# Performance work log

Measured on AMD Instinct MI355X. Metric: run time of the kernel, lower is better.

## Reference

```python
import jax, jax.numpy as jnp
import numpy as np

K = 16  # number of neighbors (init kwarg k)
N_POINTS = 8_000_000
D_FEAT = 6


def setup_inputs() -> dict:
    key = jax.random.key(0)
    k1, k2, k3 = jax.random.split(key, 3)
    P = jax.random.normal(k1, (N_POINTS, D_FEAT), dtype=jnp.float32)
    W = jax.random.normal(k2, (3, 10), dtype=jnp.float32) * 0.1  # nn.Linear(10, 3) weight
    b = jax.random.normal(k3, (3,), dtype=jnp.float32) * 0.1     # nn.Linear(10, 3) bias
    i = 12345
    return {"P": P, "W": W, "b": b, "i": i}


def reference(P, W, b, i):
    # --- knn(i): note torch .topk defaults to largest=True, so this faithfully
    # selects the K points with the LARGEST distance to point i.
    pi = P[i, :3]                                   # [3]
    d = jnp.linalg.norm(P[:, :3] - pi, axis=1)      # [N] streaming distance pass
    _, idx = jax.lax.top_k(d, K)                    # [K]
    near = P[idx]                                   # [K, D]
    nloc = near[:, :3]                              # [K, 3]

    # --- rel_pos_enc, vectorized over all K neighbors (one tiny GEMM)
    diff = pi[None, :] - nloc                       # [K, 3]
    dist = jnp.linalg.norm(diff, axis=1, keepdims=True)  # [K, 1]
    feat = jnp.concatenate(
        [jnp.broadcast_to(pi, (K, 3)), nloc, diff, dist], axis=1
    )                                               # [K, 10]
    R = feat @ W.T + b                              # [K, 3]

    # --- forward: concat neighbor coords with encoding
    return jnp.concatenate([nloc, R], axis=1)       # [K, 6]
```

## Files before the change

kernel.cpp:

```cpp
#include <hip/hip_runtime.h>
#include <math.h>

#define KTOP 16
#define T1   256
#define B1   2048
#define PTS_PER_TILE 512
#define F4_PER_TILE  768
#define T2   1024
#define NC2  (B1 * KTOP)

typedef unsigned long long ull;

__device__ __forceinline__ ull pack_key(float d, unsigned idx) {
    return ((ull)__float_as_uint(d) << 32) | (ull)(0xFFFFFFFFu - idx);
}

__device__ __forceinline__ void insert_key(ull (&k)[KTOP], ull key) {
    ull t = key;
#pragma unroll
    for (int j = 0; j < KTOP; ++j) {
        const ull a = k[j];
        const bool c = (t > a);
        k[j] = c ? t : a;
        t    = c ? a : t;
    }
}

__device__ __forceinline__ float dist3(float x, float y, float z,
                                       float px, float py, float pz) {
#pragma clang fp contract(off)
    const float dx = x - px;
    const float dy = y - py;
    const float dz = z - pz;
    const float s  = (dx * dx + dy * dy) + dz * dz;
    return sqrtf(s);
}

__global__ __launch_bounds__(T1, 4) void pass1_topk(const float* __restrict__ P,
                                                    const int*   __restrict__ ipq,
                                                    int n,
                                                    ull* __restrict__ cand) {
    __shared__ float4 tile_f4[F4_PER_TILE];

    const int tid = threadIdx.x;

    const int i0 = ipq[0];
    const float pix = P[6 * i0 + 0];
    const float piy = P[6 * i0 + 1];
    const float piz = P[6 * i0 + 2];

    ull k[KTOP];
#pragma unroll
    for (int j = 0; j < KTOP; ++j) k[j] = 0ull;

    const float4* __restrict__ P4 = (const float4*)P;
    const int nTiles = n / PTS_PER_TILE;

    int tile = blockIdx.x;
    float4 r0, r1, r2;
    if (tile < nTiles) {
        const int b = tile * F4_PER_TILE + tid;
        r0 = P4[b];
        r1 = P4[b + T1];
        r2 = P4[b + 2 * T1];
    }

    for (; tile < nTiles; tile += B1) {
        __syncthreads();
        tile_f4[tid]          = r0;
        tile_f4[tid + T1]     = r1;
        tile_f4[tid + 2 * T1] = r2;
        const int next = tile + B1;
        if (next < nTiles) {
            const int b = next * F4_PER_TILE + tid;
            r0 = P4[b];
            r1 = P4[b + T1];
            r2 = P4[b + 2 * T1];
        }
        __syncthreads();

        const float* lp = (const float*)tile_f4 + 12 * tid;
        const float x0 = lp[0], y0 = lp[1],  z0 = lp[2];
        const float x1 = lp[6], y1 = lp[7],  z1 = lp[8];
        const unsigned id0 = (unsigned)(tile * PTS_PER_TILE + 2 * tid);
        const float d0 = dist3(x0, y0, z0, pix, piy, piz);
        const float d1 = dist3(x1, y1, z1, pix, piy, piz);
        const ull k0 = pack_key(d0, id0);
        const ull k1 = pack_key(d1, id0 + 1);
        if (k0 > k[KTOP - 1]) insert_key(k, k0);
        if (k1 > k[KTOP - 1]) insert_key(k, k1);
    }

    for (int p = nTiles * PTS_PER_TILE + blockIdx.x * T1 + tid; p < n; p += B1 * T1) {
        const float d = dist3(P[6 * p], P[6 * p + 1], P[6 * p + 2], pix, piy, piz);
        const ull key = pack_key(d, (unsigned)p);
        if (key > k[KTOP - 1]) insert_key(k, key);
    }

    __shared__ ull s_w[T1 / 64];
    __shared__ ull s_best;
    const int lane = tid & 63;
    const int wid  = tid >> 6;

    for (int r = 0; r < KTOP; ++r) {
        const ull mk = k[0];
        ull rv = mk;
#pragma unroll
        for (int m = 32; m >= 1; m >>= 1) {
            const ull ov = __shfl_xor(rv, m);
            if (ov > rv) rv = ov;
        }
        if (lane == 0) s_w[wid] = rv;
        __syncthreads();
        if (tid == 0) {
            ull b = s_w[0];
            for (int w = 1; w < T1 / 64; ++w) if (s_w[w] > b) b = s_w[w];
            s_best = b;
            cand[blockIdx.x * KTOP + r] = b;
        }
        __syncthreads();
        if (mk == s_best) {
#pragma unroll
            for (int j = 0; j < KTOP - 1; ++j) k[j] = k[j + 1];
            k[KTOP - 1] = 0ull;
        }
    }
}

__global__ __launch_bounds__(T2, 1) void pass2_final(const float* __restrict__ P,
                                                     const int*   __restrict__ ipq,
                                                     const float* __restrict__ W,
                                                     const float* __restrict__ bvec,
                                                     const ull*   __restrict__ cand,
                                                     float* __restrict__ out) {
    __shared__ ull s_w[T2 / 64];
    __shared__ ull s_best;
    __shared__ ull s_final[KTOP];

    const int tid  = threadIdx.x;
    const int lane = tid & 63;
    const int wid  = tid >> 6;

    ull k[KTOP];
#pragma unroll
    for (int j = 0; j < KTOP; ++j) k[j] = 0ull;

    for (int c = tid; c < NC2; c += T2) {
        const ull key = cand[c];
        if (key > k[KTOP - 1]) insert_key(k, key);
    }

    for (int r = 0; r < KTOP; ++r) {
        const ull mk = k[0];
        ull rv = mk;
#pragma unroll
        for (int m = 32; m >= 1; m >>= 1) {
            const ull ov = __shfl_xor(rv, m);
            if (ov > rv) rv = ov;
        }
        if (lane == 0) s_w[wid] = rv;
        __syncthreads();
        if (tid == 0) {
            ull b = s_w[0];
            for (int w = 1; w < T2 / 64; ++w) if (s_w[w] > b) b = s_w[w];
            s_best = b;
            s_final[r] = b;
        }
        __syncthreads();
        if (mk == s_best) {
#pragma unroll
            for (int j = 0; j < KTOP - 1; ++j) k[j] = k[j + 1];
            k[KTOP - 1] = 0ull;
        }
    }
    __syncthreads();

    if (tid < KTOP) {
        const ull kk = s_final[tid];
        const float d = __uint_as_float((unsigned)(kk >> 32));
        const unsigned idx = 0xFFFFFFFFu - (unsigned)(kk & 0xFFFFFFFFull);
        const int   i0  = ipq[0];
        const float pix = P[6 * i0 + 0], piy = P[6 * i0 + 1], piz = P[6 * i0 + 2];
        const float nx  = P[6 * (size_t)idx + 0];
        const float ny  = P[6 * (size_t)idx + 1];
        const float nz  = P[6 * (size_t)idx + 2];
        float dx, dy, dz;
        {
#pragma clang fp contract(off)
            dx = pix - nx; dy = piy - ny; dz = piz - nz;
        }
        const float feat[10] = { pix, piy, piz, nx, ny, nz, dx, dy, dz, d };
        float R[3];
#pragma unroll
        for (int r = 0; r < 3; ++r) {
            float acc = bvec[r];
#pragma unroll
            for (int c = 0; c < 10; ++c) acc += feat[c] * W[r * 10 + c];
            R[r] = acc;
        }
        out[6 * tid + 0] = nx;   out[6 * tid + 1] = ny;   out[6 * tid + 2] = nz;
        out[6 * tid + 3] = R[0]; out[6 * tid + 4] = R[1]; out[6 * tid + 5] = R[2];
    }
}

extern "C" void kernel_launch(void* const* d_in, const int* in_sizes, int n_in,
                              void* d_out, int out_size, void* d_ws, size_t ws_size,
                              hipStream_t stream) {
    const float* P    = (const float*)d_in[0];
    const float* W    = (const float*)d_in[1];
    const float* bvec = (const float*)d_in[2];
    const int*   ipq  = (const int*)d_in[3];
    float*       out  = (float*)d_out;

    const int n = in_sizes[0] / 6;
    ull* cand = (ull*)d_ws;

    pass1_topk<<<B1, T1, 0, stream>>>(P, ipq, n, cand);
    pass2_final<<<1, T2, 0, stream>>>(P, ipq, W, bvec, cand, out);
}
```

Before: 330.5 us.

## Replace LDS tile staging with per-wavefront register shuffle decoding of point segments

```diff
diff --git a/kernel.cpp b/kernel.cpp
--- a/kernel.cpp
+++ b/kernel.cpp
@@ -4,8 +4,9 @@
 #define KTOP 16
 #define T1   256
 #define B1   2048
-#define PTS_PER_TILE 512
-#define F4_PER_TILE  768
+#define WPB  (T1 / 64)
+#define NW   (B1 * WPB)
+#define SEG  128
 #define T2   1024
 #define NC2  (B1 * KTOP)
 
@@ -40,9 +41,9 @@
                                                     const int*   __restrict__ ipq,
                                                     int n,
                                                     ull* __restrict__ cand) {
-    __shared__ float4 tile_f4[F4_PER_TILE];
-
-    const int tid = threadIdx.x;
+    const int tid  = threadIdx.x;
+    const int lane = tid & 63;
+    const int wid  = tid >> 6;
 
     const int i0 = ipq[0];
     const float pix = P[6 * i0 + 0];
@@ -54,53 +55,72 @@
     for (int j = 0; j < KTOP; ++j) k[j] = 0ull;
 
     const float4* __restrict__ P4 = (const float4*)P;
-    const int nTiles = n / PTS_PER_TILE;
-
-    int tile = blockIdx.x;
-    float4 r0, r1, r2;
-    if (tile < nTiles) {
-        const int b = tile * F4_PER_TILE + tid;
-        r0 = P4[b];
-        r1 = P4[b + T1];
-        r2 = P4[b + 2 * T1];
-    }
-
-    for (; tile < nTiles; tile += B1) {
-        __syncthreads();
-        tile_f4[tid]          = r0;
-        tile_f4[tid + T1]     = r1;
-        tile_f4[tid + 2 * T1] = r2;
-        const int next = tile + B1;
-        if (next < nTiles) {
-            const int b = next * F4_PER_TILE + tid;
-            r0 = P4[b];
-            r1 = P4[b + T1];
-            r2 = P4[b + 2 * T1];
-        }
-        __syncthreads();
-
-        const float* lp = (const float*)tile_f4 + 12 * tid;
-        const float x0 = lp[0], y0 = lp[1],  z0 = lp[2];
-        const float x1 = lp[6], y1 = lp[7],  z1 = lp[8];
-        const unsigned id0 = (unsigned)(tile * PTS_PER_TILE + 2 * tid);
-        const float d0 = dist3(x0, y0, z0, pix, piy, piz);
-        const float d1 = dist3(x1, y1, z1, pix, piy, piz);
-        const ull k0 = pack_key(d0, id0);
-        const ull k1 = pack_key(d1, id0 + 1);
+    const int nSeg = n / SEG;
+    const int gw   = blockIdx.x * WPB + wid;
+
+    const int r3 = lane % 3;
+    const int t3 = lane / 3;
+    const unsigned peOff = 2u * t3 + ((r3 == 0) ? 0u  : (r3 == 1) ? 86u : 44u);
+    const unsigned poOff = 2u * t3 + ((r3 == 0) ? 43u : (r3 == 1) ? 1u  : 87u);
+
+    for (int s = gw; s < nSeg; s += NW) {
+        const float4* __restrict__ src = P4 + (size_t)s * (3 * 64);
+        const float4 qa = src[lane];
+        const float4 qb = src[lane + 64];
+        const float4 qc = src[lane + 128];
+
+        float s0a, s0b, s0c, s1a, s1b, s1c, z2a, z2b, z2c;
+        {
+#pragma clang fp contract(off)
+            { const float dx = qa.x - pix, dy = qa.y - piy, dz = qa.z - piz;
+              s0a = (dx * dx + dy * dy) + dz * dz;
+              const float ex = qa.z - pix, ey = qa.w - piy;
+              s1a = ex * ex + ey * ey;
+              const float zz = qa.x - piz; z2a = zz * zz; }
+            { const float dx = qb.x - pix, dy = qb.y - piy, dz = qb.z - piz;
+              s0b = (dx * dx + dy * dy) + dz * dz;
+              const float ex = qb.z - pix, ey = qb.w - piy;
+              s1b = ex * ex + ey * ey;
+              const float zz = qb.x - piz; z2b = zz * zz; }
+            { const float dx = qc.x - pix, dy = qc.y - piy, dz = qc.z - piz;
+              s0c = (dx * dx + dy * dy) + dz * dz;
+              const float ex = qc.z - pix, ey = qc.w - piy;
+              s1c = ex * ex + ey * ey;
+              const float zz = qc.x - piz; z2c = zz * zz; }
+        }
+
+        const float z2na = __shfl_down(z2a, 1);
+        float       z2nb = __shfl_down(z2b, 1);
+        const float z2nc = __shfl_down(z2c, 1);
+        const float zc0  = __shfl(z2c, 0);
+        if (lane == 63) z2nb = zc0;
+
+        const float sfull = (r3 == 0) ? s0a : (r3 == 1) ? s0c : s0b;
+        const float spart = (r3 == 0) ? s1b : (r3 == 1) ? s1a : s1c;
+        const float zpart = (r3 == 0) ? z2nb : (r3 == 1) ? z2na : z2nc;
+
+        float d_e, d_o;
+        {
+#pragma clang fp contract(off)
+            d_e = sqrtf(sfull);
+            d_o = sqrtf(spart + zpart);
+        }
+
+        const unsigned base = (unsigned)s * (unsigned)SEG;
+        const ull k0 = pack_key(d_e, base + peOff);
+        const ull k1 = pack_key(d_o, base + poOff);
         if (k0 > k[KTOP - 1]) insert_key(k, k0);
         if (k1 > k[KTOP - 1]) insert_key(k, k1);
     }
 
-    for (int p = nTiles * PTS_PER_TILE + blockIdx.x * T1 + tid; p < n; p += B1 * T1) {
+    for (int p = nSeg * SEG + blockIdx.x * T1 + tid; p < n; p += B1 * T1) {
         const float d = dist3(P[6 * p], P[6 * p + 1], P[6 * p + 2], pix, piy, piz);
         const ull key = pack_key(d, (unsigned)p);
         if (key > k[KTOP - 1]) insert_key(k, key);
     }
 
-    __shared__ ull s_w[T1 / 64];
+    __shared__ ull s_w[WPB];
     __shared__ ull s_best;
-    const int lane = tid & 63;
-    const int wid  = tid >> 6;
 
     for (int r = 0; r < KTOP; ++r) {
         const ull mk = k[0];
@@ -113,10 +133,10 @@
         if (lane == 0) s_w[wid] = rv;
         __syncthreads();
         if (tid == 0) {
-            ull b = s_w[0];
-            for (int w = 1; w < T1 / 64; ++w) if (s_w[w] > b) b = s_w[w];
-            s_best = b;
-            cand[blockIdx.x * KTOP + r] = b;
+            ull bb = s_w[0];
+            for (int w = 1; w < WPB; ++w) if (s_w[w] > bb) bb = s_w[w];
+            s_best = bb;
+            cand[blockIdx.x * KTOP + r] = bb;
         }
         __syncthreads();
         if (mk == s_best) {
@@ -161,10 +181,10 @@
         if (lane == 0) s_w[wid] = rv;
         __syncthreads();
         if (tid == 0) {
-            ull b = s_w[0];
-            for (int w = 1; w < T2 / 64; ++w) if (s_w[w] > b) b = s_w[w];
-            s_best = b;
-            s_final[r] = b;
+            ull bb = s_w[0];
+            for (int w = 1; w < T2 / 64; ++w) if (s_w[w] > bb) bb = s_w[w];
+            s_best = bb;
+            s_final[r] = bb;
         }
         __syncthreads();
         if (mk == s_best) {
```

Result: no change. 331.5 us (+0.3%).
